# Optimization experiments

Hardware: AMD Instinct MI355X
Metric: run time of the kernel (lower is better)

## Reference

```python
import jax, jax.numpy as jnp
import numpy as np

B, N, CT = 64, 256, 3
HID, HEADS = 256, 4
C = HID // HEADS          # per-head channels
E = 8192                  # number of edges
NEG = 0.2                 # GATv2 leaky_relu negative slope
EPS_BN = 1e-5


def setup_inputs() -> dict:
    key = jax.random.key(0)
    ks = jax.random.split(key, 32)
    F_in = N * CT
    s1 = 1.0 / np.sqrt(F_in)
    sh = 1.0 / np.sqrt(HID)
    inp = {
        "x": jax.random.normal(ks[0], (B, N, N, CT), jnp.float32),
        "edge_index": jax.random.randint(ks[1], (2, E), 0, N, dtype=jnp.int32),
        # node_proj: Linear + BatchNorm1d (eval) params
        "W1": jax.random.normal(ks[2], (F_in, HID), jnp.float32) * s1,
        "b1": jnp.zeros((HID,), jnp.float32),
        "g1": jnp.ones((HID,), jnp.float32),
        "be1": jnp.zeros((HID,), jnp.float32),
        "m1": jnp.zeros((HID,), jnp.float32),
        "v1": jnp.ones((HID,), jnp.float32),
        # GATv2 layer 0
        "Wl0": jax.random.normal(ks[3], (HID, HID), jnp.float32) * sh,
        "bl0": jnp.zeros((HID,), jnp.float32),
        "Wr0": jax.random.normal(ks[4], (HID, HID), jnp.float32) * sh,
        "br0": jnp.zeros((HID,), jnp.float32),
        "att0": jax.random.normal(ks[5], (HEADS, C), jnp.float32) * (1.0 / np.sqrt(C)),
        "bo0": jnp.zeros((HID,), jnp.float32),
        # GATv2 layer 1
        "Wl1": jax.random.normal(ks[6], (HID, HID), jnp.float32) * sh,
        "bl1": jnp.zeros((HID,), jnp.float32),
        "Wr1": jax.random.normal(ks[7], (HID, HID), jnp.float32) * sh,
        "br1": jnp.zeros((HID,), jnp.float32),
        "att1": jax.random.normal(ks[8], (HEADS, C), jnp.float32) * (1.0 / np.sqrt(C)),
        "bo1": jnp.zeros((HID,), jnp.float32),
        # output_proj: Linear + BatchNorm1d (eval) params
        "W2": jax.random.normal(ks[9], (HID, HID), jnp.float32) * sh,
        "b2": jnp.zeros((HID,), jnp.float32),
        "g2": jnp.ones((HID,), jnp.float32),
        "be2": jnp.zeros((HID,), jnp.float32),
        "m2": jnp.zeros((HID,), jnp.float32),
        "v2": jnp.ones((HID,), jnp.float32),
    }
    return inp


def _bn(x, g, b, m, v):
    # BatchNorm1d in eval mode: per-feature affine with running stats
    return (x - m) * jax.lax.rsqrt(v + EPS_BN) * g + b


def _gatv2(h, src, dst, Wl, bl, Wr, br, att, bo):
    # h: (N, HID). GATv2Conv (PyG semantics): lin_l on source, lin_r on target.
    xl = (h @ Wl + bl).reshape(N, HEADS, C)
    xr = (h @ Wr + br).reshape(N, HEADS, C)
    x_j = xl[src]                        # (E, H, C) source features
    x_i = xr[dst]                        # (E, H, C) target features
    e = jax.nn.leaky_relu(x_i + x_j, NEG)
    logits = jnp.einsum('ehc,hc->eh', e, att)          # (E, H)
    mx = jax.ops.segment_max(logits, dst, num_segments=N)
    a = jnp.exp(logits - mx[dst])
    den = jax.ops.segment_sum(a, dst, num_segments=N)
    a = a / (den[dst] + 1e-16)                         # neighborhood softmax
    out = jax.ops.segment_sum(x_j * a[:, :, None], dst, num_segments=N)
    return out.reshape(N, HID) + bo


def reference(x, edge_index, W1, b1, g1, be1, m1, v1,
              Wl0, bl0, Wr0, br0, att0, bo0,
              Wl1, bl1, Wr1, br1, att1, bo1,
              W2, b2, g2, be2, m2, v2):
    gelu = lambda t: jax.nn.gelu(t, approximate=False)
    xf = x.reshape(B, N, N * CT)
    # node_proj (eval: dropout off, BN uses running stats -> vmappable)
    h = gelu(_bn(xf @ W1 + b1, g1, be1, m1, v1))       # (B, N, HID)
    src, dst = edge_index[0], edge_index[1]

    def per_sample(hn):
        h0 = gelu(_gatv2(hn, src, dst, Wl0, bl0, Wr0, br0, att0, bo0))
        h1 = gelu(_gatv2(h0, src, dst, Wl1, bl1, Wr1, br1, att1, bo1))
        return h1.mean(axis=0)                          # mean over nodes

    pooled = jax.vmap(per_sample)(h)                    # (B, HID)
    return gelu(_bn(pooled @ W2 + b2, g2, be2, m2, v2))
```

## Files before the change

### kernel.cpp

```cpp
#include <hip/hip_runtime.h>
#include <hip/hip_bf16.h>
#include <math.h>

#define BATCH   64
#define NNODES  256
#define HID     256
#define HEADS   4
#define CDIM    64
#define NEDGES  8192
#define NEG_SLOPE 0.2f
#define EPS_BN 1e-5f


typedef __bf16 bf16_t;
typedef __bf16 bf16x8 __attribute__((ext_vector_type(8)));
typedef float  f32x4  __attribute__((ext_vector_type(4)));

__device__ __forceinline__ float gelu_f(float x) {
    return 0.5f * x * (1.0f + erff(x * 0.70710678118654752440f));
}

#define SWZ(r, c) ((c) ^ ((r) & 3) ^ (((r) >> 2) & 3) ^ (((r) >> 4) & 3))

__global__ __launch_bounds__(256, 4) void np_gemm(
        const float* __restrict__ x, const float* __restrict__ W1,
        const float* __restrict__ b1, const float* __restrict__ g1,
        const float* __restrict__ be1, const float* __restrict__ m1,
        const float* __restrict__ v1, bf16_t* __restrict__ H) {
    __shared__ bf16_t As[2][32 * 32];
    __shared__ bf16_t Bs[2][256 * 32];
    const int K = 768;
    const int tid  = threadIdx.x;
    const int lane = tid & 63;
    const int wv   = tid >> 6;
    const int mblk = blockIdx.x * 32;

    f32x4 acc[2][4];
    #pragma unroll
    for (int f = 0; f < 2; ++f)
        #pragma unroll
        for (int t = 0; t < 4; ++t) acc[f][t] = (f32x4){0.f, 0.f, 0.f, 0.f};

    const int arow = (tid & 127) >> 2;
    const int achk = tid & 3;
    const int gr   = mblk + arow;
    const int arr  = (gr & 63) * 256 + (gr >> 6);
    const int fm   = lane & 15, q = lane >> 4;
    const int nq   = tid & 63;
    const int kg   = tid >> 6;

    f32x4 a0, a1;
    f32x4 bw[8];

    if (tid < 128) {
        const float* ap = x + (size_t)arr * K + achk * 8;
        a0 = *(const f32x4*)ap; a1 = *(const f32x4*)(ap + 4);
    }
    {
        const float* wp = W1 + (size_t)(kg * 8) * 256 + nq * 4;
        #pragma unroll
        for (int j = 0; j < 8; ++j) bw[j] = *(const f32x4*)(wp + j * 256);
    }

    #pragma unroll
    for (int kt = 0; kt < 24; ++kt) {
        const int buf = kt & 1;
        if (tid < 128) {
            bf16x8 v;
            #pragma unroll
            for (int j = 0; j < 4; ++j) { v[j] = (bf16_t)a0[j]; v[4 + j] = (bf16_t)a1[j]; }
            *(bf16x8*)(&As[buf][(arow * 4 + SWZ(arow, achk)) * 8]) = v;
        }
        #pragma unroll
        for (int i = 0; i < 4; ++i) {
            const int n = nq * 4 + i;
            bf16x8 v;
            #pragma unroll
            for (int j = 0; j < 8; ++j) v[j] = (bf16_t)bw[j][i];
            *(bf16x8*)(&Bs[buf][(n * 4 + SWZ(n, kg)) * 8]) = v;
        }
        __syncthreads();
        if (kt + 1 < 24) {
            const int k0 = (kt + 1) * 32;
            if (tid < 128) {
                const float* ap = x + (size_t)arr * K + k0 + achk * 8;
                a0 = *(const f32x4*)ap; a1 = *(const f32x4*)(ap + 4);
            }
            const float* wp = W1 + (size_t)(k0 + kg * 8) * 256 + nq * 4;
            #pragma unroll
            for (int j = 0; j < 8; ++j) bw[j] = *(const f32x4*)(wp + j * 256);
        }
        bf16x8 af[2], bfv[4];
        #pragma unroll
        for (int f = 0; f < 2; ++f) {
            const int r = f * 16 + fm;
            af[f] = *(const bf16x8*)(&As[buf][(r * 4 + SWZ(r, q)) * 8]);
        }
        #pragma unroll
        for (int t = 0; t < 4; ++t) {
            const int n = wv * 64 + t * 16 + fm;
            bfv[t] = *(const bf16x8*)(&Bs[buf][(n * 4 + SWZ(n, q)) * 8]);
        }
        #pragma unroll
        for (int f = 0; f < 2; ++f)
            #pragma unroll
            for (int t = 0; t < 4; ++t)
                acc[f][t] = __builtin_amdgcn_mfma_f32_16x16x32_bf16(
                    af[f], bfv[t], acc[f][t], 0, 0, 0);
    }

    const int quad = lane >> 4, cn = lane & 15;
    #pragma unroll
    for (int t = 0; t < 4; ++t) {
        const int n = wv * 64 + t * 16 + cn;
        const float s = g1[n] * rsqrtf(v1[n] + EPS_BN);
        const float shift = (b1[n] - m1[n]) * s + be1[n];
        #pragma unroll
        for (int f = 0; f < 2; ++f) {
            #pragma unroll
            for (int r = 0; r < 4; ++r) {
                const int m = mblk + f * 16 + quad * 4 + r;
                H[(size_t)m * 256 + n] = (bf16_t)gelu_f(acc[f][t][r] * s + shift);
            }
        }
    }
}

__global__ __launch_bounds__(256) void prep_kernel(
        const int* __restrict__ ei,
        const float* __restrict__ Wa, const float* __restrict__ Wb,
        const float* __restrict__ Wc, const float* __restrict__ Wd,
        int* __restrict__ noff, int* __restrict__ csrc,
        bf16_t* __restrict__ Ta, bf16_t* __restrict__ Tb,
        bf16_t* __restrict__ Tc, bf16_t* __restrict__ Td) {
    const int bx = blockIdx.x;
    const int tid = threadIdx.x;
    if (bx == 256) {
        __shared__ int cnt[NNODES];
        __shared__ int sc[NNODES];
        cnt[tid] = 0;
        __syncthreads();
        for (int e = tid; e < NEDGES; e += 256) atomicAdd(&cnt[ei[NEDGES + e]], 1);
        __syncthreads();
        sc[tid] = cnt[tid];
        __syncthreads();
        #pragma unroll
        for (int ofs = 1; ofs < 256; ofs <<= 1) {
            const int t = (tid >= ofs) ? sc[tid - ofs] : 0;
            __syncthreads();
            sc[tid] += t;
            __syncthreads();
        }
        const int excl = sc[tid] - cnt[tid];
        noff[tid] = excl;
        if (tid == 255) noff[NNODES] = sc[255];
        cnt[tid] = excl;
        __syncthreads();
        for (int e = tid; e < NEDGES; e += 256) {
            int d = ei[NEDGES + e];
            int p = atomicAdd(&cnt[d], 1);
            csrc[p] = ei[e];
        }
        return;
    }
    __shared__ float tile[32][33];
    const int mid = bx >> 6, t = bx & 63;
    const float* in; bf16_t* out;
    if (mid == 0) { in = Wa; out = Ta; }
    else if (mid == 1) { in = Wb; out = Tb; }
    else if (mid == 2) { in = Wc; out = Tc; }
    else { in = Wd; out = Td; }
    const int kt = t >> 3, nt = t & 7;
    const int k0 = kt * 32, n0 = nt * 32;
    const int x = tid & 31, y = tid >> 5;
    #pragma unroll
    for (int j = 0; j < 4; ++j)
        tile[y + j * 8][x] = in[(size_t)(k0 + y + j * 8) * 256 + n0 + x];
    __syncthreads();
    #pragma unroll
    for (int j = 0; j < 4; ++j) {
        const int n = n0 + y + j * 8;
        out[((size_t)kt * 256 + n) * 32 + x] = (bf16_t)tile[x][y + j * 8];
    }
}

template<int KTILES>
__global__ __launch_bounds__(256, 4) void gemm_kernel(
        const bf16_t* __restrict__ Ap,
        const bf16_t* __restrict__ Bt0, const bf16_t* __restrict__ Bt1,
        bf16_t* __restrict__ C0p, bf16_t* __restrict__ C1p,
        const float* __restrict__ bias0, const float* __restrict__ bias1) {
    __shared__ bf16_t As[2][32 * 32];
    __shared__ bf16_t Bs[2][256 * 32];
    const int K = KTILES * 32;
    const int tid  = threadIdx.x;
    const int lane = tid & 63;
    const int wv   = tid >> 6;
    const int mblk = blockIdx.y * 32;
    const bool second = (blockIdx.x == 1);
    const bf16_t* Bt = second ? Bt1 : Bt0;
    bf16_t* Cp = second ? C1p : C0p;
    const float* bias = second ? bias1 : bias0;

    f32x4 acc[2][4];
    #pragma unroll
    for (int f = 0; f < 2; ++f)
        #pragma unroll
        for (int t = 0; t < 4; ++t) acc[f][t] = (f32x4){0.f, 0.f, 0.f, 0.f};

    const int arow = (tid & 127) >> 2;
    const int achk = tid & 3;
    const int fm   = lane & 15, q = lane >> 4;
    const int bn   = tid >> 2;

    bf16x8 aReg; bf16x8 bReg[4];
    if (tid < 128)
        aReg = *(const bf16x8*)(Ap + (size_t)(mblk + arow) * K + achk * 8);
    {
        const bf16_t* panel = Bt + (size_t)tid * 8;
        #pragma unroll
        for (int c = 0; c < 4; ++c) bReg[c] = *(const bf16x8*)(panel + c * 2048);
    }

    #pragma unroll
    for (int kt = 0; kt < KTILES; ++kt) {
        const int buf = kt & 1;
        if (tid < 128)
            *(bf16x8*)(&As[buf][(arow * 4 + SWZ(arow, achk)) * 8]) = aReg;
        #pragma unroll
        for (int c = 0; c < 4; ++c) {
            const int n = c * 64 + bn;
            *(bf16x8*)(&Bs[buf][(n * 4 + SWZ(n, achk)) * 8]) = bReg[c];
        }
        __syncthreads();
        if (kt + 1 < KTILES) {
            const int k0 = (kt + 1) * 32;
            if (tid < 128)
                aReg = *(const bf16x8*)(Ap + (size_t)(mblk + arow) * K + k0 + achk * 8);
            const bf16_t* panel = Bt + (size_t)(kt + 1) * (256 * 32) + (size_t)tid * 8;
            #pragma unroll
            for (int c = 0; c < 4; ++c) bReg[c] = *(const bf16x8*)(panel + c * 2048);
        }
        bf16x8 af[2], bfv[4];
        #pragma unroll
        for (int f = 0; f < 2; ++f) {
            const int r = f * 16 + fm;
            af[f] = *(const bf16x8*)(&As[buf][(r * 4 + SWZ(r, q)) * 8]);
        }
        #pragma unroll
        for (int t = 0; t < 4; ++t) {
            const int n = wv * 64 + t * 16 + fm;
            bfv[t] = *(const bf16x8*)(&Bs[buf][(n * 4 + SWZ(n, q)) * 8]);
        }
        #pragma unroll
        for (int f = 0; f < 2; ++f)
            #pragma unroll
            for (int t = 0; t < 4; ++t)
                acc[f][t] = __builtin_amdgcn_mfma_f32_16x16x32_bf16(
                    af[f], bfv[t], acc[f][t], 0, 0, 0);
    }

    const int quad = lane >> 4, cn = lane & 15;
    #pragma unroll
    for (int t = 0; t < 4; ++t) {
        const int n = wv * 64 + t * 16 + cn;
        const float bv = bias[n];
        #pragma unroll
        for (int f = 0; f < 2; ++f) {
            #pragma unroll
            for (int r = 0; r < 4; ++r) {
                const int m = mblk + f * 16 + quad * 4 + r;
                Cp[(size_t)m * 256 + n] = (bf16_t)(acc[f][t][r] + bv);
            }
        }
    }
}

__global__ __launch_bounds__(256) void edge_kernel(
        const bf16_t* __restrict__ XL, const bf16_t* __restrict__ XR,
        const float* __restrict__ att, const float* __restrict__ bo,
        const int* __restrict__ noff, const int* __restrict__ csrc,
        bf16_t* __restrict__ Hout) {
    const int bid  = blockIdx.x;
    const int i    = bid >> 3;
    const int tid  = threadIdx.x;
    const int w    = tid >> 6;
    const int lane = tid & 63;
    const int bg   = lane >> 3;
    const int cg   = lane & 7;
    const int b    = (bid & 7) * 8 + bg;
    const int cbase = w * CDIM + cg * 8;
    const size_t orow = ((size_t)i * BATCH + b) * HID + cbase;
    const float* bor = bo + cbase;

    const int s0 = noff[i], s1 = noff[i + 1];
    if (s0 == s1) {
        bf16x8 ov;
        #pragma unroll
        for (int q = 0; q < 8; ++q) ov[q] = (bf16_t)gelu_f(bor[q]);
        *(bf16x8*)(Hout + orow) = ov;
        return;
    }

    float a6[8], a4[8], xi[8];
    {
        const float* ar = att + cbase;
        const bf16x8 xr = *(const bf16x8*)(XR + orow);
        #pragma unroll
        for (int q = 0; q < 8; ++q) {
            float a = ar[q];
            a6[q] = 0.6f * a; a4[q] = 0.4f * a;
            xi[q] = (float)xr[q];
        }
    }

    const bf16_t* XLb = XL + (size_t)b * HID + cbase;
    const size_t RSTR = (size_t)BATCH * HID;

    float dA = 0.f, dB = 0.f;
    float accA[8], accB[8];
    #pragma unroll
    for (int q = 0; q < 8; ++q) { accA[q] = 0.f; accB[q] = 0.f; }

    int jA = csrc[s0];
    int jB = csrc[(s0 + 1 < s1) ? s0 + 1 : s0];
    bf16x8 xA = *(const bf16x8*)(XLb + (size_t)jA * RSTR);
    bf16x8 xB = *(const bf16x8*)(XLb + (size_t)jB * RSTR);

    for (int e = s0; e < s1; e += 2) {
        const int nA = (e + 2 < s1) ? e + 2 : s0;
        const int nB = (e + 3 < s1) ? e + 3 : s0;
        const int jnA = csrc[nA], jnB = csrc[nB];
        const bf16x8 xnA = *(const bf16x8*)(XLb + (size_t)jnA * RSTR);
        const bf16x8 xnB = *(const bf16x8*)(XLb + (size_t)jnB * RSTR);

        float fA[8], fB[8];
        #pragma unroll
        for (int q = 0; q < 8; ++q) { fA[q] = (float)xA[q]; fB[q] = (float)xB[q]; }
        float pA0 = 0.f, pA1 = 0.f, pB0 = 0.f, pB1 = 0.f;
        #pragma unroll
        for (int q = 0; q < 8; q += 2) {
            const float zA0 = xi[q] + fA[q],     zB0 = xi[q] + fB[q];
            const float zA1 = xi[q+1] + fA[q+1], zB1 = xi[q+1] + fB[q+1];
            pA0 = fmaf(a6[q], zA0, pA0);     pA0 = fmaf(a4[q], __builtin_fabsf(zA0), pA0);
            pA1 = fmaf(a6[q+1], zA1, pA1);   pA1 = fmaf(a4[q+1], __builtin_fabsf(zA1), pA1);
            pB0 = fmaf(a6[q], zB0, pB0);     pB0 = fmaf(a4[q], __builtin_fabsf(zB0), pB0);
            pB1 = fmaf(a6[q+1], zB1, pB1);   pB1 = fmaf(a4[q+1], __builtin_fabsf(zB1), pB1);
        }
        float pA = pA0 + pA1, pB = pB0 + pB1;
        pA += __shfl_xor(pA, 1, 64);  pB += __shfl_xor(pB, 1, 64);
        pA += __shfl_xor(pA, 2, 64);  pB += __shfl_xor(pB, 2, 64);
        pA += __shfl_xor(pA, 4, 64);  pB += __shfl_xor(pB, 4, 64);

        const float wA = __expf(pA);
        const float wB = ((e + 1 < s1) ? 1.f : 0.f) * __expf(pB);
        dA += wA; dB += wB;
        #pragma unroll
        for (int q = 0; q < 8; ++q) {
            accA[q] = fmaf(wA, fA[q], accA[q]);
            accB[q] = fmaf(wB, fB[q], accB[q]);
        }
        xA = xnA; xB = xnB;
    }

    const float inv = 1.0f / (dA + dB + 1e-16f);
    bf16x8 ov;
    #pragma unroll
    for (int q = 0; q < 8; ++q) {
        const float o = (accA[q] + accB[q]) * inv + bor[q];
        ov[q] = (bf16_t)gelu_f(o);
    }
    *(bf16x8*)(Hout + orow) = ov;
}

__global__ __launch_bounds__(256) void pf_kernel(
        const bf16_t* __restrict__ H1, const float* __restrict__ W2,
        const float* __restrict__ b2, const float* __restrict__ g2,
        const float* __restrict__ be2, const float* __restrict__ m2,
        const float* __restrict__ v2, float* __restrict__ out) {
    __shared__ float pl[HID];
    const int b = blockIdx.x, f = threadIdx.x;
    float s = 0.f;
    for (int n = 0; n < NNODES; ++n)
        s += (float)H1[((size_t)n * BATCH + b) * HID + f];
    pl[f] = s * (1.0f / (float)NNODES);
    __syncthreads();
    float acc = 0.f;
    for (int k = 0; k < HID; ++k) acc += pl[k] * W2[(size_t)k * HID + f];
    acc += b2[f];
    const float scale = g2[f] * rsqrtf(v2[f] + EPS_BN);
    acc = (acc - m2[f]) * scale + be2[f];
    out[b * HID + f] = gelu_f(acc);
}

extern "C" void kernel_launch(void* const* d_in, const int* in_sizes, int n_in,
                              void* d_out, int out_size, void* d_ws, size_t ws_size,
                              hipStream_t stream) {
    const float* x    = (const float*)d_in[0];
    const int*   ei   = (const int*)d_in[1];
    const float* W1   = (const float*)d_in[2];
    const float* b1   = (const float*)d_in[3];
    const float* g1   = (const float*)d_in[4];
    const float* be1  = (const float*)d_in[5];
    const float* m1   = (const float*)d_in[6];
    const float* v1   = (const float*)d_in[7];
    const float* Wl0  = (const float*)d_in[8];
    const float* bl0  = (const float*)d_in[9];
    const float* Wr0  = (const float*)d_in[10];
    const float* br0  = (const float*)d_in[11];
    const float* att0 = (const float*)d_in[12];
    const float* bo0  = (const float*)d_in[13];
    const float* Wl1  = (const float*)d_in[14];
    const float* bl1  = (const float*)d_in[15];
    const float* Wr1  = (const float*)d_in[16];
    const float* br1  = (const float*)d_in[17];
    const float* att1 = (const float*)d_in[18];
    const float* bo1  = (const float*)d_in[19];
    const float* W2   = (const float*)d_in[20];
    const float* b2   = (const float*)d_in[21];
    const float* g2   = (const float*)d_in[22];
    const float* be2  = (const float*)d_in[23];
    const float* m2   = (const float*)d_in[24];
    const float* v2   = (const float*)d_in[25];

    char* ws = (char*)d_ws;
    const int M = BATCH * NNODES;
    const size_t SZ_BF = (size_t)M * HID * sizeof(bf16_t);

    int*    noff = (int*)ws;                ws += 2048;
    int*    csrc = (int*)ws;                ws += 32768;
    bf16_t* Wl0t = (bf16_t*)ws;             ws += 256 * 256 * 2;
    bf16_t* Wr0t = (bf16_t*)ws;             ws += 256 * 256 * 2;
    bf16_t* Wl1t = (bf16_t*)ws;             ws += 256 * 256 * 2;
    bf16_t* Wr1t = (bf16_t*)ws;             ws += 256 * 256 * 2;
    bf16_t* H    = (bf16_t*)ws;             ws += SZ_BF;
    bf16_t* H2   = (bf16_t*)ws;             ws += SZ_BF;
    bf16_t* XL   = (bf16_t*)ws;             ws += SZ_BF;
    bf16_t* XR   = (bf16_t*)ws;             ws += SZ_BF;

    np_gemm<<<512, 256, 0, stream>>>(x, W1, b1, g1, be1, m1, v1, H);

    prep_kernel<<<257, 256, 0, stream>>>(ei, Wl0, Wr0, Wl1, Wr1,
                                         noff, csrc, Wl0t, Wr0t, Wl1t, Wr1t);

    gemm_kernel<8><<<dim3(2, 512), 256, 0, stream>>>(
        H, Wl0t, Wr0t, XL, XR, bl0, br0);
    edge_kernel<<<NNODES * 8, 256, 0, stream>>>(XL, XR, att0, bo0, noff, csrc, H2);

    gemm_kernel<8><<<dim3(2, 512), 256, 0, stream>>>(
        H2, Wl1t, Wr1t, XL, XR, bl1, br1);
    edge_kernel<<<NNODES * 8, 256, 0, stream>>>(XL, XR, att1, bo1, noff, csrc, H);

    pf_kernel<<<BATCH, 256, 0, stream>>>(H, W2, b2, g2, be2, m2, v2, (float*)d_out);
}
```

Baseline: 291.9 us.

## Vectorize edge kernel with packed f32x2 math and split pooling into two kernels

The edge kernel now unpacks bf16 pairs with bit shifts into float2 vectors and computes leaky-ReLU as max(z, 0.2z), using packed float2 multiply-adds in place of scalar FMAs and fabs. The final pooling is split into a 256-block partial-sum kernel plus a small final projection kernel, replacing a 64-block kernel that looped serially over 256 nodes. This targets VALU instruction count in the edge loop and poor parallelism in the pooling tail, at the cost of one extra launch and a small workspace buffer.

Result: faster. 281.8 us (-3.5%).

```diff
diff --git a/kernel.cpp b/kernel.cpp
--- a/kernel.cpp
+++ b/kernel.cpp
@@ -15,9 +15,27 @@
 typedef __bf16 bf16_t;
 typedef __bf16 bf16x8 __attribute__((ext_vector_type(8)));
 typedef float  f32x4  __attribute__((ext_vector_type(4)));
+typedef float  f32x2  __attribute__((ext_vector_type(2)));
+typedef unsigned int u32;
+typedef u32 u32x4v __attribute__((ext_vector_type(4)));
 
 __device__ __forceinline__ float gelu_f(float x) {
     return 0.5f * x * (1.0f + erff(x * 0.70710678118654752440f));
+}
+
+__device__ __forceinline__ f32x2 vmax2(f32x2 a, f32x2 b) {
+#if __has_builtin(__builtin_elementwise_max)
+    return __builtin_elementwise_max(a, b);
+#else
+    f32x2 r; r[0] = fmaxf(a[0], b[0]); r[1] = fmaxf(a[1], b[1]); return r;
+#endif
+}
+
+__device__ __forceinline__ f32x2 unpk(u32 u) {
+    f32x2 f;
+    f[0] = __builtin_bit_cast(float, u << 16);
+    f[1] = __builtin_bit_cast(float, u & 0xffff0000u);
+    return f;
 }
 
 #define SWZ(r, c) ((c) ^ ((r) & 3) ^ (((r) >> 2) & 3) ^ (((r) >> 4) & 3))
@@ -302,15 +320,13 @@
         return;
     }
 
-    float a6[8], a4[8], xi[8];
+    f32x2 att2[4], xi2[4];
     {
-        const float* ar = att + cbase;
-        const bf16x8 xr = *(const bf16x8*)(XR + orow);
-        #pragma unroll
-        for (int q = 0; q < 8; ++q) {
-            float a = ar[q];
-            a6[q] = 0.6f * a; a4[q] = 0.4f * a;
-            xi[q] = (float)xr[q];
+        const u32x4v xr = *(const u32x4v*)(XR + orow);
+        #pragma unroll
+        for (int k = 0; k < 4; ++k) {
+            att2[k] = *(const f32x2*)(att + cbase + 2 * k);
+            xi2[k]  = unpk(xr[k]);
         }
     }
 
@@ -318,36 +334,40 @@
     const size_t RSTR = (size_t)BATCH * HID;
 
     float dA = 0.f, dB = 0.f;
-    float accA[8], accB[8];
-    #pragma unroll
-    for (int q = 0; q < 8; ++q) { accA[q] = 0.f; accB[q] = 0.f; }
+    f32x2 accA[4], accB[4];
+    #pragma unroll
+    for (int k = 0; k < 4; ++k) {
+        accA[k] = (f32x2){0.f, 0.f};
+        accB[k] = (f32x2){0.f, 0.f};
+    }
 
     int jA = csrc[s0];
     int jB = csrc[(s0 + 1 < s1) ? s0 + 1 : s0];
-    bf16x8 xA = *(const bf16x8*)(XLb + (size_t)jA * RSTR);
-    bf16x8 xB = *(const bf16x8*)(XLb + (size_t)jB * RSTR);
+    u32x4v uA = *(const u32x4v*)(XLb + (size_t)jA * RSTR);
+    u32x4v uB = *(const u32x4v*)(XLb + (size_t)jB * RSTR);
 
     for (int e = s0; e < s1; e += 2) {
         const int nA = (e + 2 < s1) ? e + 2 : s0;
         const int nB = (e + 3 < s1) ? e + 3 : s0;
         const int jnA = csrc[nA], jnB = csrc[nB];
-        const bf16x8 xnA = *(const bf16x8*)(XLb + (size_t)jnA * RSTR);
-        const bf16x8 xnB = *(const bf16x8*)(XLb + (size_t)jnB * RSTR);
-
-        float fA[8], fB[8];
-        #pragma unroll
-        for (int q = 0; q < 8; ++q) { fA[q] = (float)xA[q]; fB[q] = (float)xB[q]; }
-        float pA0 = 0.f, pA1 = 0.f, pB0 = 0.f, pB1 = 0.f;
-        #pragma unroll
-        for (int q = 0; q < 8; q += 2) {
-            const float zA0 = xi[q] + fA[q],     zB0 = xi[q] + fB[q];
-            const float zA1 = xi[q+1] + fA[q+1], zB1 = xi[q+1] + fB[q+1];
-            pA0 = fmaf(a6[q], zA0, pA0);     pA0 = fmaf(a4[q], __builtin_fabsf(zA0), pA0);
-            pA1 = fmaf(a6[q+1], zA1, pA1);   pA1 = fmaf(a4[q+1], __builtin_fabsf(zA1), pA1);
-            pB0 = fmaf(a6[q], zB0, pB0);     pB0 = fmaf(a4[q], __builtin_fabsf(zB0), pB0);
-            pB1 = fmaf(a6[q+1], zB1, pB1);   pB1 = fmaf(a4[q+1], __builtin_fabsf(zB1), pB1);
-        }
-        float pA = pA0 + pA1, pB = pB0 + pB1;
+        const u32x4v unA = *(const u32x4v*)(XLb + (size_t)jnA * RSTR);
+        const u32x4v unB = *(const u32x4v*)(XLb + (size_t)jnB * RSTR);
+
+        f32x2 fA[4], fB[4];
+        f32x2 pA2 = (f32x2){0.f, 0.f}, pB2 = (f32x2){0.f, 0.f};
+        #pragma unroll
+        for (int k = 0; k < 4; ++k) {
+            fA[k] = unpk(uA[k]);
+            fB[k] = unpk(uB[k]);
+            const f32x2 zA = xi2[k] + fA[k];
+            const f32x2 zB = xi2[k] + fB[k];
+            const f32x2 mA = vmax2(zA, zA * 0.2f);
+            const f32x2 mB = vmax2(zB, zB * 0.2f);
+            pA2 += att2[k] * mA;
+            pB2 += att2[k] * mB;
+        }
+        float pA = pA2[0] + pA2[1];
+        float pB = pB2[0] + pB2[1];
         pA += __shfl_xor(pA, 1, 64);  pB += __shfl_xor(pB, 1, 64);
         pA += __shfl_xor(pA, 2, 64);  pB += __shfl_xor(pB, 2, 64);
         pA += __shfl_xor(pA, 4, 64);  pB += __shfl_xor(pB, 4, 64);
@@ -355,42 +375,55 @@
         const float wA = __expf(pA);
         const float wB = ((e + 1 < s1) ? 1.f : 0.f) * __expf(pB);
         dA += wA; dB += wB;
-        #pragma unroll
-        for (int q = 0; q < 8; ++q) {
-            accA[q] = fmaf(wA, fA[q], accA[q]);
-            accB[q] = fmaf(wB, fB[q], accB[q]);
-        }
-        xA = xnA; xB = xnB;
+        const f32x2 wA2 = (f32x2){wA, wA};
+        const f32x2 wB2 = (f32x2){wB, wB};
+        #pragma unroll
+        for (int k = 0; k < 4; ++k) {
+            accA[k] += wA2 * fA[k];
+            accB[k] += wB2 * fB[k];
+        }
+        uA = unA; uB = unB;
     }
 
     const float inv = 1.0f / (dA + dB + 1e-16f);
     bf16x8 ov;
     #pragma unroll
-    for (int q = 0; q < 8; ++q) {
-        const float o = (accA[q] + accB[q]) * inv + bor[q];
-        ov[q] = (bf16_t)gelu_f(o);
+    for (int k = 0; k < 4; ++k) {
+        const f32x2 bo2 = *(const f32x2*)(bor + 2 * k);
+        const f32x2 o2 = (accA[k] + accB[k]) * inv + bo2;
+        ov[2 * k]     = (bf16_t)gelu_f(o2[0]);
+        ov[2 * k + 1] = (bf16_t)gelu_f(o2[1]);
     }
     *(bf16x8*)(Hout + orow) = ov;
 }
 
-__global__ __launch_bounds__(256) void pf_kernel(
-        const bf16_t* __restrict__ H1, const float* __restrict__ W2,
+__global__ __launch_bounds__(256) void pool_kernel(const bf16_t* __restrict__ H1,
+                                                   float* __restrict__ P) {
+    const int b = blockIdx.x, c = blockIdx.y, f = threadIdx.x;
+    const bf16_t* p = H1 + ((size_t)(c * 64) * BATCH + b) * HID + f;
+    float s = 0.f;
+    for (int n = 0; n < 64; ++n) s += (float)p[(size_t)n * BATCH * HID];
+    P[((size_t)b * 4 + c) * HID + f] = s;
+}
+
+__global__ __launch_bounds__(256) void final_kernel(
+        const float* __restrict__ P, const float* __restrict__ W2,
         const float* __restrict__ b2, const float* __restrict__ g2,
         const float* __restrict__ be2, const float* __restrict__ m2,
         const float* __restrict__ v2, float* __restrict__ out) {
     __shared__ float pl[HID];
     const int b = blockIdx.x, f = threadIdx.x;
+    float s4 = 0.f;
+    #pragma unroll
+    for (int c = 0; c < 4; ++c) s4 += P[((size_t)b * 4 + c) * HID + f];
+    pl[f] = s4 * (1.0f / (float)NNODES);
+    __syncthreads();
     float s = 0.f;
-    for (int n = 0; n < NNODES; ++n)
-        s += (float)H1[((size_t)n * BATCH + b) * HID + f];
-    pl[f] = s * (1.0f / (float)NNODES);
-    __syncthreads();
-    float acc = 0.f;
-    for (int k = 0; k < HID; ++k) acc += pl[k] * W2[(size_t)k * HID + f];
-    acc += b2[f];
+    for (int k = 0; k < HID; ++k) s += pl[k] * W2[(size_t)k * HID + f];
+    s += b2[f];
     const float scale = g2[f] * rsqrtf(v2[f] + EPS_BN);
-    acc = (acc - m2[f]) * scale + be2[f];
-    out[b * HID + f] = gelu_f(acc);
+    s = (s - m2[f]) * scale + be2[f];
+    out[b * HID + f] = gelu_f(s);
 }
 
 extern "C" void kernel_launch(void* const* d_in, const int* in_sizes, int n_in,
@@ -437,6 +470,7 @@
     bf16_t* H2   = (bf16_t*)ws;             ws += SZ_BF;
     bf16_t* XL   = (bf16_t*)ws;             ws += SZ_BF;
     bf16_t* XR   = (bf16_t*)ws;             ws += SZ_BF;
+    float*  P    = (float*)ws;              ws += BATCH * 4 * HID * 4;
 
     np_gemm<<<512, 256, 0, stream>>>(x, W1, b1, g1, be1, m1, v1, H);
 
@@ -451,5 +485,7 @@
         H2, Wl1t, Wr1t, XL, XR, bl1, br1);
     edge_kernel<<<NNODES * 8, 256, 0, stream>>>(XL, XR, att1, bo1, noff, csrc, H);
 
-    pf_kernel<<<BATCH, 256, 0, stream>>>(H, W2, b2, g2, be2, m2, v2, (float*)d_out);
-}
+    pool_kernel<<<dim3(BATCH, 4), 256, 0, stream>>>(H, P);
+    final_kernel<<<BATCH, 256, 0, stream>>>(P, W2, b2, g2, be2, m2, v2,
+                                            (float*)d_out);
+}
```
